# Kernel tuning notes

Measured on AMD Instinct MI355X. Metric: run time of the kernel, lower is better.

Reference implementation:

```python
import jax, jax.numpy as jnp
import numpy as np

HEAD_SIZE = 64


def setup_inputs() -> dict:
    key = jax.random.key(0)
    k1, k2, k3, k4 = jax.random.split(key, 4)
    B, T, C = 4, 4096, 1024
    x = jax.random.normal(k1, (B, T, C), dtype=jnp.float32)
    s = 1.0 / np.sqrt(C)  # ~kaiming-uniform scale for Linear weights
    Wk = jax.random.normal(k2, (C, HEAD_SIZE), dtype=jnp.float32) * s
    Wq = jax.random.normal(k3, (C, HEAD_SIZE), dtype=jnp.float32) * s
    Wv = jax.random.normal(k4, (C, HEAD_SIZE), dtype=jnp.float32) * s
    return {"x": x, "Wk": Wk, "Wq": Wq, "Wv": Wv}


def reference(x, Wk, Wq, Wv):
    # x: [B,T,C]; Wk/Wq/Wv: [C,H]
    B, T, C = x.shape
    H = Wk.shape[1]
    k = jnp.einsum('btc,ch->bth', x, Wk)
    q = jnp.einsum('btc,ch->bth', x, Wq)
    v = jnp.einsum('btc,ch->bth', x, Wv)
    scale = 1.0 / jnp.sqrt(jnp.asarray(H, dtype=x.dtype))
    scores = jnp.einsum('bqh,bkh->bqk', q, k) * scale  # [B,T,T]
    causal = jnp.tril(jnp.ones((T, T), dtype=bool))
    scores = jnp.where(causal, scores, jnp.asarray(-jnp.inf, dtype=scores.dtype))
    attn = jax.nn.softmax(scores, axis=-1)
    out = jnp.einsum('bqk,bkh->bqh', attn, v)  # [B,T,H]
    return out
```

## Files before the change

### kernel.cpp

```cpp
#include <hip/hip_runtime.h>
#include <hip/hip_bf16.h>

#define T_ 4096
#define C_ 1024
#define H_ 64
#define LSTR 72
#define XBS 1032

typedef short bf16x8 __attribute__((ext_vector_type(8)));
typedef float f32x4 __attribute__((ext_vector_type(4)));

__device__ __forceinline__ short f2bf(float f) {
  union { __hip_bfloat16 h; short s; } u;
  u.h = __float2bfloat16(f);
  return u.s;
}
__device__ __forceinline__ unsigned pack2(float a, float b) {
  return ((unsigned)(unsigned short)f2bf(b) << 16) | (unsigned short)f2bf(a);
}

__global__ void wtrans_kernel(const float* __restrict__ Wk,
                              const float* __restrict__ Wq,
                              const float* __restrict__ Wv,
                              __hip_bfloat16* __restrict__ Wtf) {
  int tid = blockIdx.x * 256 + threadIdx.x;
  const int j = tid & 7;
  const int lane = (tid >> 3) & 63;
  const int m = lane & 15;
  const int quad = lane >> 4;
  const int f = (tid >> 9) & 15;
  const int nt = f & 3;
  const int ks = f >> 2;
  const int c = (tid >> 13) & 7;
  const int which = tid >> 16;
  const float* W = (which == 0) ? Wk : ((which == 1) ? Wq : Wv);
  const int cc = c * 128 + ks * 32 + quad * 8 + j;
  const int h = nt * 16 + m;
  Wtf[tid] = __float2bfloat16(W[cc * 64 + h]);
}

__global__ __launch_bounds__(256) void proj_kernel(
    const float* __restrict__ x, const __hip_bfloat16* __restrict__ Wtf,
    __hip_bfloat16* __restrict__ qb, __hip_bfloat16* __restrict__ Kf,
    __hip_bfloat16* __restrict__ Vf) {
  __shared__ __hip_bfloat16 Xb[16 * XBS];
  const int tid = threadIdx.x;
  const int lane = tid & 63;
  const int wave = tid >> 6;
  const int m = lane & 15;
  const int quad = lane >> 4;
  const int bid = blockIdx.x;
  const int bb0 = (bid & 7) >> 1;
  const int tile = ((bid >> 3) << 1) + (bid & 1);
  const int t0 = bb0 * T_ + tile * 16;

  const float4* xtile = (const float4*)(x + (size_t)t0 * C_);
  float4 xv[16];
#pragma unroll
  for (int k = 0; k < 16; ++k) xv[k] = xtile[tid + k * 256];
#pragma unroll
  for (int k = 0; k < 16; ++k) {
    const int idx = tid + k * 256;
    const int row = idx >> 8;
    const int c4 = idx & 255;
    uint2 u = {pack2(xv[k].x, xv[k].y), pack2(xv[k].z, xv[k].w)};
    *(uint2*)(&Xb[row * XBS + c4 * 4]) = u;
  }
  __syncthreads();

  int whichs[3], ntls[3];
  const __hip_bfloat16* wb[3];
#pragma unroll
  for (int i = 0; i < 3; ++i) {
    const int g = wave * 3 + i;
    whichs[i] = g >> 2;
    ntls[i] = g & 3;
    wb[i] = Wtf + (size_t)whichs[i] * 65536 + ntls[i] * 512 + lane * 8;
  }
  f32x4 acc[3];
#pragma unroll
  for (int i = 0; i < 3; ++i) acc[i] = (f32x4){0.f, 0.f, 0.f, 0.f};

#pragma unroll
  for (int c = 0; c < 8; ++c) {
    bf16x8 bq[12];
#pragma unroll
    for (int i = 0; i < 3; ++i)
#pragma unroll
      for (int ks = 0; ks < 4; ++ks)
        bq[i * 4 + ks] = *(const bf16x8*)(wb[i] + (c * 16 + ks * 4) * 512);
#pragma unroll
    for (int ks = 0; ks < 4; ++ks) {
      bf16x8 a = *(const bf16x8*)(&Xb[m * XBS + c * 128 + ks * 32 + quad * 8]);
#pragma unroll
      for (int i = 0; i < 3; ++i)
        acc[i] = __builtin_amdgcn_mfma_f32_16x16x32_bf16(a, bq[i * 4 + ks],
                                                         acc[i], 0, 0, 0);
    }
  }

  const int bb = t0 >> 12;
  const int tloc = t0 & (T_ - 1);
  const int ktile = tloc >> 6;
  const float cscale = 0.18033688011112042f;

#pragma unroll
  for (int i = 0; i < 3; ++i) {
    const int which = whichs[i];
    const int ntl = ntls[i];
    if (which == 1) {
#pragma unroll
      for (int r = 0; r < 4; ++r)
        qb[(size_t)(t0 + quad * 4 + r) * H_ + ntl * 16 + m] =
            __float2bfloat16(acc[i][r] * cscale);
    } else if (which == 0) {
      __hip_bfloat16* dst = Kf + ((size_t)bb * 64 + ktile) * 4096;
      const int ntK = (tloc >> 4) & 3;
      const int wh = ntl >> 1;
      const int quadK = (ntl * 2 + (m >> 3)) & 3;
      const int j = m & 7;
#pragma unroll
      for (int r = 0; r < 4; ++r) {
        const int mK = quad * 4 + r;
        dst[(ntK * 2 + wh) * 512 + (quadK * 16 + mK) * 8 + j] =
            __float2bfloat16(acc[i][r]);
      }
    } else {
      __hip_bfloat16* dst = Vf + ((size_t)bb * 64 + ktile) * 4096;
#pragma unroll
      for (int r = 0; r < 4; ++r) {
        const int kvo = (tloc & 63) + quad * 4 + r;
        const int half = (kvo >> 5) & 1;
        const int quadV = (kvo >> 3) & 3;
        const int j = kvo & 7;
        dst[(ntl * 2 + half) * 512 + (quadV * 16 + m) * 8 + j] =
            __float2bfloat16(acc[i][r]);
      }
    }
  }
}

__global__ __launch_bounds__(256, 4) void fa_pass1(
    const __hip_bfloat16* __restrict__ qg, const __hip_bfloat16* __restrict__ Kf,
    const __hip_bfloat16* __restrict__ Vf, float* __restrict__ Opart,
    float* __restrict__ Ml) {
  __shared__ __hip_bfloat16 Pl[4][16 * LSTR];
  const int lane = threadIdx.x & 63;
  const int wave = threadIdx.x >> 6;
  const int m = lane & 15;
  const int quad = lane >> 4;

  const int bid = blockIdx.x;
  const int xcd = bid & 7;
  const int b = xcd >> 1;
  const int pb = ((bid >> 3) << 1) + (xcd & 1);
  const int j2 = 1151 - (pb * 4 + wave);
  const int jid = b * 1152 + j2;
  int g = 7;
  while (16 * g * (g + 1) > j2) --g;
  const int r2 = j2 - 16 * g * (g + 1);
  const int qt = 32 * g + r2 / (g + 1);
  const int c = r2 - (r2 / (g + 1)) * (g + 1);
  const int q0 = qt * 16;
  const int k0s = c * 512;
  const int kend0 = k0s + 512;
  const int kend = (kend0 < q0 + 16) ? kend0 : (q0 + 16);
  const int ntile = (kend - k0s + 63) >> 6;

  const __hip_bfloat16* qbase = qg + ((size_t)b * T_ + q0 + m) * H_;
  bf16x8 qf0 = *(const bf16x8*)(qbase + quad * 8);
  bf16x8 qf1 = *(const bf16x8*)(qbase + 32 + quad * 8);

  f32x4 Oacc[4];
#pragma unroll
  for (int i = 0; i < 4; ++i) Oacc[i] = (f32x4){0.f, 0.f, 0.f, 0.f};
  float psum = 0.f;

  const __hip_bfloat16* kgf = Kf + (size_t)b * 262144 + lane * 8;
  const __hip_bfloat16* vgf = Vf + (size_t)b * 262144 + lane * 8;
  __hip_bfloat16* Plw = &Pl[wave][0];

  for (int it = 0; it < ntile; ++it) {
    const int ktile = (k0s >> 6) + it;
    const int k0 = ktile * 64;
    const __hip_bfloat16* kp = kgf + (size_t)ktile * 4096;
    const __hip_bfloat16* vp = vgf + (size_t)ktile * 4096;

    f32x4 s[4];
#pragma unroll
    for (int nt = 0; nt < 4; ++nt) {
      bf16x8 kf0 = *(const bf16x8*)(kp + nt * 1024);
      bf16x8 kf1 = *(const bf16x8*)(kp + nt * 1024 + 512);
      f32x4 t = (f32x4){0.f, 0.f, 0.f, 0.f};
      t = __builtin_amdgcn_mfma_f32_16x16x32_bf16(kf0, qf0, t, 0, 0, 0);
      t = __builtin_amdgcn_mfma_f32_16x16x32_bf16(kf1, qf1, t, 0, 0, 0);
      s[nt] = t;
    }
    bf16x8 vf[8];
#pragma unroll
    for (int nt = 0; nt < 4; ++nt) {
      vf[2 * nt] = *(const bf16x8*)(vp + nt * 1024);
      vf[2 * nt + 1] = *(const bf16x8*)(vp + nt * 1024 + 512);
    }

    const bool needmask = (k0 + 63 > q0);
#pragma unroll
    for (int nt = 0; nt < 4; ++nt) {
      float p[4];
#pragma unroll
      for (int r = 0; r < 4; ++r) {
        float sv = s[nt][r];
        if (needmask && (k0 + nt * 16 + quad * 4 + r) > (q0 + m))
          sv = -__builtin_inff();
        p[r] = exp2f(sv);
        psum += p[r];
      }
      uint2 u = {pack2(p[0], p[1]), pack2(p[2], p[3])};
      *(uint2*)(&Plw[m * LSTR + nt * 16 + quad * 4]) = u;
    }

    bf16x8 pf0 = *(const bf16x8*)(&Plw[m * LSTR + quad * 8]);
    bf16x8 pf1 = *(const bf16x8*)(&Plw[m * LSTR + 32 + quad * 8]);
#pragma unroll
    for (int nt = 0; nt < 4; ++nt) {
      Oacc[nt] = __builtin_amdgcn_mfma_f32_16x16x32_bf16(pf0, vf[2 * nt], Oacc[nt], 0, 0, 0);
      Oacc[nt] = __builtin_amdgcn_mfma_f32_16x16x32_bf16(pf1, vf[2 * nt + 1], Oacc[nt], 0, 0, 0);
    }
  }

  psum += __shfl_xor(psum, 16);
  psum += __shfl_xor(psum, 32);

  float* Op = Opart + (size_t)jid * 1024;
#pragma unroll
  for (int nt = 0; nt < 4; ++nt)
#pragma unroll
    for (int r = 0; r < 4; ++r)
      __builtin_nontemporal_store(Oacc[nt][r],
                                  &Op[(quad * 4 + r) * 64 + nt * 16 + m]);
  if (lane < 16) __builtin_nontemporal_store(psum, &Ml[(size_t)jid * 16 + lane]);
}

__global__ __launch_bounds__(256) void fa_combine(
    const float* __restrict__ Opart, const float* __restrict__ Ml,
    float* __restrict__ out) {
  const int bq = blockIdx.x;
  const int b = bq >> 8;
  const int qt = bq & 255;
  const int g = qt >> 5;
  const int nc = g + 1;
  const int jbase = b * 1152 + 16 * g * (g + 1) + (qt & 31) * nc;
  const int r = threadIdx.x >> 4;
  const int h0 = (threadIdx.x & 15) * 4;

  float4 O = {0.f, 0.f, 0.f, 0.f};
  float L = 0.f;
  for (int c = 0; c < nc; ++c) {
    L += Ml[(size_t)(jbase + c) * 16 + r];
    float4 o = *(const float4*)(Opart + (size_t)(jbase + c) * 1024 + r * 64 + h0);
    O.x += o.x; O.y += o.y; O.z += o.z; O.w += o.w;
  }
  float inv = 1.f / L;
  float4 res = {O.x * inv, O.y * inv, O.z * inv, O.w * inv};
  *(float4*)(out + ((size_t)b * T_ + qt * 16 + r) * H_ + h0) = res;
}

extern "C" void kernel_launch(void* const* d_in, const int* in_sizes, int n_in,
                              void* d_out, int out_size, void* d_ws, size_t ws_size,
                              hipStream_t stream) {
  const float* x = (const float*)d_in[0];
  const float* Wk = (const float*)d_in[1];
  const float* Wq = (const float*)d_in[2];
  const float* Wv = (const float*)d_in[3];
  float* out = (float*)d_out;
  char* ws = (char*)d_ws;
  __hip_bfloat16* Wtf = (__hip_bfloat16*)ws;
  __hip_bfloat16* qb = (__hip_bfloat16*)(ws + 393216);
  __hip_bfloat16* Kf = (__hip_bfloat16*)(ws + 2490368);
  __hip_bfloat16* Vf = (__hip_bfloat16*)(ws + 4587520);
  float* Opart = (float*)(ws + 6684672);
  float* Ml = (float*)(ws + 25559040);

  hipLaunchKernelGGL(wtrans_kernel, dim3(768), dim3(256), 0, stream, Wk, Wq, Wv, Wtf);
  hipLaunchKernelGGL(proj_kernel, dim3(1024), dim3(256), 0, stream, x, Wtf, qb, Kf, Vf);
  hipLaunchKernelGGL(fa_pass1, dim3(1152), dim3(256), 0, stream, qb, Kf, Vf, Opart, Ml);
  hipLaunchKernelGGL(fa_combine, dim3(1024), dim3(256), 0, stream, Opart, Ml, out);
}
```

Before: 145.2 us.

## Process two query tiles per wave to reuse K/V fragments in attention pass

Each wave now handles two adjacent 16-row query tiles (32 queries) against a chunk of up to four key tiles, loading each K and V fragment once and using it for both query tiles. The work decomposition, partial-output layout, combine indexing and workspace offsets are changed to match, and the launch bound drops to 3 blocks per CU to make room for the doubled accumulators. This is meant to halve global K/V load traffic per MFMA. In exchange it raises register pressure, lowers occupancy and shrinks the chunk size, which adds more partials to combine.

```diff
diff --git a/kernel.cpp b/kernel.cpp
--- a/kernel.cpp
+++ b/kernel.cpp
@@ -140,11 +140,11 @@
   }
 }
 
-__global__ __launch_bounds__(256, 4) void fa_pass1(
+__global__ __launch_bounds__(256, 3) void fa_pass1(
     const __hip_bfloat16* __restrict__ qg, const __hip_bfloat16* __restrict__ Kf,
     const __hip_bfloat16* __restrict__ Vf, float* __restrict__ Opart,
     float* __restrict__ Ml) {
-  __shared__ __hip_bfloat16 Pl[4][16 * LSTR];
+  __shared__ __hip_bfloat16 Pl[4][2][16 * LSTR];
   const int lane = threadIdx.x & 63;
   const int wave = threadIdx.x >> 6;
   const int m = lane & 15;
@@ -154,47 +154,67 @@
   const int xcd = bid & 7;
   const int b = xcd >> 1;
   const int pb = ((bid >> 3) << 1) + (xcd & 1);
-  const int j2 = 1151 - (pb * 4 + wave);
-  const int jid = b * 1152 + j2;
-  int g = 7;
-  while (16 * g * (g + 1) > j2) --g;
-  const int r2 = j2 - 16 * g * (g + 1);
-  const int qt = 32 * g + r2 / (g + 1);
+  const int j2 = 1087 - (pb * 4 + wave);
+  const int jid = b * 1088 + j2;
+
+  int g = 15;
+  while (4 * g * (g + 1) > j2) --g;
+  const int r2 = j2 - 4 * g * (g + 1);
+  const int u = 8 * g + r2 / (g + 1);
   const int c = r2 - (r2 / (g + 1)) * (g + 1);
-  const int q0 = qt * 16;
-  const int k0s = c * 512;
-  const int kend0 = k0s + 512;
-  const int kend = (kend0 < q0 + 16) ? kend0 : (q0 + 16);
-  const int ntile = (kend - k0s + 63) >> 6;
-
-  const __hip_bfloat16* qbase = qg + ((size_t)b * T_ + q0 + m) * H_;
-  bf16x8 qf0 = *(const bf16x8*)(qbase + quad * 8);
-  bf16x8 qf1 = *(const bf16x8*)(qbase + 32 + quad * 8);
-
-  f32x4 Oacc[4];
-#pragma unroll
-  for (int i = 0; i < 4; ++i) Oacc[i] = (f32x4){0.f, 0.f, 0.f, 0.f};
-  float psum = 0.f;
+  const int ntile_u = (u >> 1) + 1;
+  const int kt0 = 4 * c;
+  const int kc = ntile_u - kt0;
+  const int kcount = (kc < 4) ? kc : 4;
+  const int q0a = u * 32;
+  const int q0b = q0a + 16;
+
+  const __hip_bfloat16* qbaseA = qg + ((size_t)b * T_ + q0a + m) * H_;
+  const __hip_bfloat16* qbaseB = qg + ((size_t)b * T_ + q0b + m) * H_;
+  bf16x8 qa0 = *(const bf16x8*)(qbaseA + quad * 8);
+  bf16x8 qa1 = *(const bf16x8*)(qbaseA + 32 + quad * 8);
+  bf16x8 qb0 = *(const bf16x8*)(qbaseB + quad * 8);
+  bf16x8 qb1 = *(const bf16x8*)(qbaseB + 32 + quad * 8);
+
+  f32x4 OaccA[4], OaccB[4];
+#pragma unroll
+  for (int i = 0; i < 4; ++i) {
+    OaccA[i] = (f32x4){0.f, 0.f, 0.f, 0.f};
+    OaccB[i] = (f32x4){0.f, 0.f, 0.f, 0.f};
+  }
+  float psumA = 0.f, psumB = 0.f;
 
   const __hip_bfloat16* kgf = Kf + (size_t)b * 262144 + lane * 8;
   const __hip_bfloat16* vgf = Vf + (size_t)b * 262144 + lane * 8;
-  __hip_bfloat16* Plw = &Pl[wave][0];
-
-  for (int it = 0; it < ntile; ++it) {
-    const int ktile = (k0s >> 6) + it;
+  __hip_bfloat16* PlA = &Pl[wave][0][0];
+  __hip_bfloat16* PlB = &Pl[wave][1][0];
+
+  for (int it = 0; it < kcount; ++it) {
+    const int ktile = kt0 + it;
     const int k0 = ktile * 64;
     const __hip_bfloat16* kp = kgf + (size_t)ktile * 4096;
     const __hip_bfloat16* vp = vgf + (size_t)ktile * 4096;
 
-    f32x4 s[4];
-#pragma unroll
-    for (int nt = 0; nt < 4; ++nt) {
-      bf16x8 kf0 = *(const bf16x8*)(kp + nt * 1024);
-      bf16x8 kf1 = *(const bf16x8*)(kp + nt * 1024 + 512);
+    bf16x8 kf[8];
+#pragma unroll
+    for (int nt = 0; nt < 4; ++nt) {
+      kf[2 * nt] = *(const bf16x8*)(kp + nt * 1024);
+      kf[2 * nt + 1] = *(const bf16x8*)(kp + nt * 1024 + 512);
+    }
+    f32x4 sA[4], sB[4];
+#pragma unroll
+    for (int nt = 0; nt < 4; ++nt) {
       f32x4 t = (f32x4){0.f, 0.f, 0.f, 0.f};
-      t = __builtin_amdgcn_mfma_f32_16x16x32_bf16(kf0, qf0, t, 0, 0, 0);
-      t = __builtin_amdgcn_mfma_f32_16x16x32_bf16(kf1, qf1, t, 0, 0, 0);
-      s[nt] = t;
+      t = __builtin_amdgcn_mfma_f32_16x16x32_bf16(kf[2 * nt], qa0, t, 0, 0, 0);
+      t = __builtin_amdgcn_mfma_f32_16x16x32_bf16(kf[2 * nt + 1], qa1, t, 0, 0, 0);
+      sA[nt] = t;
+    }
+#pragma unroll
+    for (int nt = 0; nt < 4; ++nt) {
+      f32x4 t = (f32x4){0.f, 0.f, 0.f, 0.f};
+      t = __builtin_amdgcn_mfma_f32_16x16x32_bf16(kf[2 * nt], qb0, t, 0, 0, 0);
+      t = __builtin_amdgcn_mfma_f32_16x16x32_bf16(kf[2 * nt + 1], qb1, t, 0, 0, 0);
+      sB[nt] = t;
     }
     bf16x8 vf[8];
 #pragma unroll
@@ -203,42 +223,70 @@
       vf[2 * nt + 1] = *(const bf16x8*)(vp + nt * 1024 + 512);
     }
 
-    const bool needmask = (k0 + 63 > q0);
+    const bool maskA = (k0 + 63 > q0a);
 #pragma unroll
     for (int nt = 0; nt < 4; ++nt) {
       float p[4];
 #pragma unroll
       for (int r = 0; r < 4; ++r) {
-        float sv = s[nt][r];
-        if (needmask && (k0 + nt * 16 + quad * 4 + r) > (q0 + m))
+        float sv = sA[nt][r];
+        if (maskA && (k0 + nt * 16 + quad * 4 + r) > (q0a + m))
           sv = -__builtin_inff();
         p[r] = exp2f(sv);
-        psum += p[r];
+        psumA += p[r];
       }
-      uint2 u = {pack2(p[0], p[1]), pack2(p[2], p[3])};
-      *(uint2*)(&Plw[m * LSTR + nt * 16 + quad * 4]) = u;
-    }
-
-    bf16x8 pf0 = *(const bf16x8*)(&Plw[m * LSTR + quad * 8]);
-    bf16x8 pf1 = *(const bf16x8*)(&Plw[m * LSTR + 32 + quad * 8]);
-#pragma unroll
-    for (int nt = 0; nt < 4; ++nt) {
-      Oacc[nt] = __builtin_amdgcn_mfma_f32_16x16x32_bf16(pf0, vf[2 * nt], Oacc[nt], 0, 0, 0);
-      Oacc[nt] = __builtin_amdgcn_mfma_f32_16x16x32_bf16(pf1, vf[2 * nt + 1], Oacc[nt], 0, 0, 0);
-    }
-  }
-
-  psum += __shfl_xor(psum, 16);
-  psum += __shfl_xor(psum, 32);
-
-  float* Op = Opart + (size_t)jid * 1024;
+      uint2 pu = {pack2(p[0], p[1]), pack2(p[2], p[3])};
+      *(uint2*)(&PlA[m * LSTR + nt * 16 + quad * 4]) = pu;
+    }
+    const bool maskB = (k0 + 63 > q0b);
+#pragma unroll
+    for (int nt = 0; nt < 4; ++nt) {
+      float p[4];
+#pragma unroll
+      for (int r = 0; r < 4; ++r) {
+        float sv = sB[nt][r];
+        if (maskB && (k0 + nt * 16 + quad * 4 + r) > (q0b + m))
+          sv = -__builtin_inff();
+        p[r] = exp2f(sv);
+        psumB += p[r];
+      }
+      uint2 pu = {pack2(p[0], p[1]), pack2(p[2], p[3])};
+      *(uint2*)(&PlB[m * LSTR + nt * 16 + quad * 4]) = pu;
+    }
+
+    bf16x8 pa0 = *(const bf16x8*)(&PlA[m * LSTR + quad * 8]);
+    bf16x8 pa1 = *(const bf16x8*)(&PlA[m * LSTR + 32 + quad * 8]);
+    bf16x8 pb0 = *(const bf16x8*)(&PlB[m * LSTR + quad * 8]);
+    bf16x8 pb1 = *(const bf16x8*)(&PlB[m * LSTR + 32 + quad * 8]);
+#pragma unroll
+    for (int nt = 0; nt < 4; ++nt) {
+      OaccA[nt] = __builtin_amdgcn_mfma_f32_16x16x32_bf16(pa0, vf[2 * nt], OaccA[nt], 0, 0, 0);
+      OaccA[nt] = __builtin_amdgcn_mfma_f32_16x16x32_bf16(pa1, vf[2 * nt + 1], OaccA[nt], 0, 0, 0);
+      OaccB[nt] = __builtin_amdgcn_mfma_f32_16x16x32_bf16(pb0, vf[2 * nt], OaccB[nt], 0, 0, 0);
+      OaccB[nt] = __builtin_amdgcn_mfma_f32_16x16x32_bf16(pb1, vf[2 * nt + 1], OaccB[nt], 0, 0, 0);
+    }
+  }
+
+  psumA += __shfl_xor(psumA, 16);
+  psumA += __shfl_xor(psumA, 32);
+  psumB += __shfl_xor(psumB, 16);
+  psumB += __shfl_xor(psumB, 32);
+
+  float* OpA = Opart + (size_t)jid * 2048;
+  float* OpB = OpA + 1024;
 #pragma unroll
   for (int nt = 0; nt < 4; ++nt)
 #pragma unroll
-    for (int r = 0; r < 4; ++r)
-      __builtin_nontemporal_store(Oacc[nt][r],
-                                  &Op[(quad * 4 + r) * 64 + nt * 16 + m]);
-  if (lane < 16) __builtin_nontemporal_store(psum, &Ml[(size_t)jid * 16 + lane]);
+    for (int r = 0; r < 4; ++r) {
+      __builtin_nontemporal_store(OaccA[nt][r],
+                                  &OpA[(quad * 4 + r) * 64 + nt * 16 + m]);
+      __builtin_nontemporal_store(OaccB[nt][r],
+                                  &OpB[(quad * 4 + r) * 64 + nt * 16 + m]);
+    }
+  if (lane < 16) {
+    __builtin_nontemporal_store(psumA, &Ml[(size_t)jid * 32 + lane]);
+    __builtin_nontemporal_store(psumB, &Ml[(size_t)jid * 32 + 16 + lane]);
+  }
 }
 
 __global__ __launch_bounds__(256) void fa_combine(
@@ -247,17 +295,20 @@
   const int bq = blockIdx.x;
   const int b = bq >> 8;
   const int qt = bq & 255;
-  const int g = qt >> 5;
+  const int u = qt >> 1;
+  const int g = u >> 3;
   const int nc = g + 1;
-  const int jbase = b * 1152 + 16 * g * (g + 1) + (qt & 31) * nc;
+  const int sel = qt & 1;
+  const int jbase = b * 1088 + 4 * g * (g + 1) + (u - 8 * g) * (g + 1);
   const int r = threadIdx.x >> 4;
   const int h0 = (threadIdx.x & 15) * 4;
 
   float4 O = {0.f, 0.f, 0.f, 0.f};
   float L = 0.f;
   for (int c = 0; c < nc; ++c) {
-    L += Ml[(size_t)(jbase + c) * 16 + r];
-    float4 o = *(const float4*)(Opart + (size_t)(jbase + c) * 1024 + r * 64 + h0);
+    L += Ml[(size_t)(jbase + c) * 32 + sel * 16 + r];
+    float4 o = *(const float4*)(Opart + (size_t)(jbase + c) * 2048 + sel * 1024 +
+                                r * 64 + h0);
     O.x += o.x; O.y += o.y; O.z += o.z; O.w += o.w;
   }
   float inv = 1.f / L;
@@ -279,10 +330,10 @@
   __hip_bfloat16* Kf = (__hip_bfloat16*)(ws + 2490368);
   __hip_bfloat16* Vf = (__hip_bfloat16*)(ws + 4587520);
   float* Opart = (float*)(ws + 6684672);
-  float* Ml = (float*)(ws + 25559040);
+  float* Ml = (float*)(ws + 42336256);
 
   hipLaunchKernelGGL(wtrans_kernel, dim3(768), dim3(256), 0, stream, Wk, Wq, Wv, Wtf);
   hipLaunchKernelGGL(proj_kernel, dim3(1024), dim3(256), 0, stream, x, Wtf, qb, Kf, Vf);
-  hipLaunchKernelGGL(fa_pass1, dim3(1152), dim3(256), 0, stream, qb, Kf, Vf, Opart, Ml);
+  hipLaunchKernelGGL(fa_pass1, dim3(1088), dim3(256), 0, stream, qb, Kf, Vf, Opart, Ml);
   hipLaunchKernelGGL(fa_combine, dim3(1024), dim3(256), 0, stream, Opart, Ml, out);
 }
```

New measurement: 155.7 us. 7.2% more time.
